# Kernel tuning notes

Measured on AMD Instinct MI355X. Metric: run time of the kernel, lower is better.

The kernel has to match this reference:

```python
import jax, jax.numpy as jnp
import numpy as np

NEG_INF_SCALE = -1e9  # matches mask * -1000000000.0 in the original


def setup_inputs() -> dict:
    key = jax.random.key(0)
    k1, k2, k3, k4 = jax.random.split(key, 4)
    B, H, S, D = 2, 16, 2048, 64
    return {
        "query": jax.random.normal(k1, (B, H, S, D), dtype=jnp.float32),
        "key": jax.random.normal(k2, (B, H, S, D), dtype=jnp.float32),
        "value": jax.random.normal(k3, (B, H, S, D), dtype=jnp.float32),
        "mask": jax.random.randint(k4, (B, 1, 1, S), 0, 2, dtype=jnp.int32),
    }


def reference(query, key, value, mask):
    head_dimension = query.shape[-1]
    scale = 1.0 / jnp.sqrt(jnp.float32(head_dimension))
    # (b h q d),(b h k d) -> (b h q k)
    logits = jnp.einsum("bhqd,bhkd->bhqk", query, key) * scale
    logits = logits + mask.astype(logits.dtype) * NEG_INF_SCALE
    attention_weights = jax.nn.softmax(logits, axis=-1)
    # (b h q k),(b h k d) -> (b h q d)
    output = jnp.einsum("bhqk,bhkd->bhqd", attention_weights, value)
    return output, attention_weights
```

## Files before the change

### kernel.cpp

```cpp
#include <hip/hip_runtime.h>

#define SEQ   2048
#define DIM   64
#define NB    2
#define NH    16
#define NHEAD (NB * NH)
#define BQ    128
#define BK    64
#define NKT   (SEQ / BK)
#define NQT   (SEQ / BQ)
#define QSCALE 0.18033688011112042f

typedef float  f32x4  __attribute__((ext_vector_type(4)));
typedef short  bf16x8 __attribute__((ext_vector_type(8)));
typedef short  s16x4  __attribute__((ext_vector_type(4)));
typedef unsigned short u16;
typedef u16    u16x8  __attribute__((ext_vector_type(8)));
typedef unsigned int u32x4 __attribute__((ext_vector_type(4)));

__device__ __forceinline__ short f2bf(float x) {
    unsigned u = __float_as_uint(x);
    return (short)((u + 0x7FFFu + ((u >> 16) & 1u)) >> 16);
}

__device__ __forceinline__ unsigned cvtpk(float lo, float hi) {
    unsigned r;
    asm("v_cvt_pk_bf16_f32 %0, %1, %2" : "=v"(r) : "v"(lo), "v"(hi));
    return r;
}

__device__ __forceinline__ void gll16(const void* g, void* l) {
    __builtin_amdgcn_global_load_lds(
        (const __attribute__((address_space(1))) unsigned int*)g,
        (__attribute__((address_space(3))) unsigned int*)l, 16, 0, 0);
}

__device__ __forceinline__ bf16x8 ldfrag_swz(const u16* tile, int row, int kbase) {
    const char* rp = (const char*)(tile + row * 64);
    const int sw = (row & 7) << 4;
    s16x4 lo = *reinterpret_cast<const s16x4*>(rp + (((kbase << 1)     ) ^ sw));
    s16x4 hi = *reinterpret_cast<const s16x4*>(rp + (((kbase << 1) + 32) ^ sw));
    bf16x8 f;
    f[0] = lo[0]; f[1] = lo[1]; f[2] = lo[2]; f[3] = lo[3];
    f[4] = hi[0]; f[5] = hi[1]; f[6] = hi[2]; f[7] = hi[3];
    return f;
}

__global__ __launch_bounds__(256)
void conv_k_kernel(const float* __restrict__ K, u16* __restrict__ Kp)
{
    const int idx = (int)blockIdx.x * 256 + (int)threadIdx.x;
    const int u  = idx & 7;
    const int r  = (idx >> 3) & 63;
    const int kt = (idx >> 9) & 31;
    const int h  = idx >> 14;
    const int d0 = ((u ^ (r & 7)) << 3);
    const float* src = K + (((size_t)h * SEQ + (size_t)kt * 64 + r) * DIM + d0);
    const float4 a = *reinterpret_cast<const float4*>(src);
    const float4 b = *reinterpret_cast<const float4*>(src + 4);
    u16x8 o;
    o[0] = (u16)f2bf(a.x); o[1] = (u16)f2bf(a.y); o[2] = (u16)f2bf(a.z); o[3] = (u16)f2bf(a.w);
    o[4] = (u16)f2bf(b.x); o[5] = (u16)f2bf(b.y); o[6] = (u16)f2bf(b.z); o[7] = (u16)f2bf(b.w);
    *reinterpret_cast<u16x8*>(Kp + (size_t)idx * 8) = o;
}

__global__ __launch_bounds__(256)
void conv_v_kernel(const float* __restrict__ V, u16* __restrict__ Vp)
{
    __shared__ float tile[64][65];
    const int tid = (int)threadIdx.x;
    const int h   = (int)blockIdx.x >> 5;
    const int kt  = (int)blockIdx.x & 31;

    const int row0 = tid >> 4;
    const int c0   = (tid & 15) << 2;
    #pragma unroll
    for (int i = 0; i < 4; ++i) {
        const int row = row0 + (i << 4);
        const float4 v = *reinterpret_cast<const float4*>(
            V + (((size_t)h * SEQ + (size_t)kt * 64 + row) * DIM + c0));
        tile[row][c0 + 0] = v.x; tile[row][c0 + 1] = v.y;
        tile[row][c0 + 2] = v.z; tile[row][c0 + 3] = v.w;
    }
    __syncthreads();

    #pragma unroll
    for (int i = 0; i < 2; ++i) {
        const int oi = tid + i * 256;
        const int u  = oi & 7;
        const int rd = oi >> 3;
        const int k0 = ((u ^ (rd & 7)) << 3);
        u16x8 o;
        #pragma unroll
        for (int j = 0; j < 8; ++j)
            o[j] = (u16)f2bf(tile[k0 + j][rd]);
        *reinterpret_cast<u16x8*>(Vp + ((size_t)((h * 32 + kt) * 512 + oi)) * 8) = o;
    }
}

__global__ __launch_bounds__(512, 4)
void sdpa_main_kernel(const float* __restrict__ Qp, const u16* __restrict__ Kp,
                      const u16* __restrict__ Vp, const int* __restrict__ Mp,
                      float* __restrict__ Op, float* __restrict__ Pg_)
{
    __shared__ u16   Ks[2][4096];
    __shared__ u16   Vs[2][4096];
    __shared__ float Fb[SEQ];

    const int tid  = (int)threadIdx.x;
    const int lane = tid & 63;
    const int w    = tid >> 6;
    const int mrow = lane & 15;
    const int kgrp = (lane >> 4) << 2;

    const int bid  = (int)blockIdx.x;
    const int xcd  = bid & 7;
    const int slot = bid >> 3;
    const int bh   = xcd * 4 + (slot >> 4);
    const int qt   = slot & 15;

    const size_t headoff = (size_t)bh * SEQ * DIM;
    const float* Qg = Qp + headoff + (size_t)qt * BQ * DIM;
    const u16*   Kh = Kp + (size_t)bh * NKT * 4096;
    const u16*   Vh = Vp + (size_t)bh * NKT * 4096;
    const int*   Mg = Mp + (size_t)(bh / NH) * SEQ;
    float*       Og = Op + headoff + (size_t)qt * BQ * DIM;
    float*       Pg = Pg_ + ((size_t)bh * SEQ + (size_t)qt * BQ) * SEQ;

    {
        const int4 m0 = *reinterpret_cast<const int4*>(Mg + tid * 4);
        float4 f0;
        f0.x = m0.x ? -1.0e9f : 0.0f; f0.y = m0.y ? -1.0e9f : 0.0f;
        f0.z = m0.z ? -1.0e9f : 0.0f; f0.w = m0.w ? -1.0e9f : 0.0f;
        *reinterpret_cast<float4*>(&Fb[tid * 4]) = f0;
    }

    bf16x8 qf0, qf1;
    {
        const float* qrow = Qg + (size_t)(w * 16 + mrow) * DIM;
        const float4 a = *reinterpret_cast<const float4*>(qrow + kgrp);
        const float4 b = *reinterpret_cast<const float4*>(qrow + 16 + kgrp);
        const float4 c = *reinterpret_cast<const float4*>(qrow + 32 + kgrp);
        const float4 d = *reinterpret_cast<const float4*>(qrow + 48 + kgrp);
        qf0[0] = f2bf(a.x * QSCALE); qf0[1] = f2bf(a.y * QSCALE);
        qf0[2] = f2bf(a.z * QSCALE); qf0[3] = f2bf(a.w * QSCALE);
        qf0[4] = f2bf(b.x * QSCALE); qf0[5] = f2bf(b.y * QSCALE);
        qf0[6] = f2bf(b.z * QSCALE); qf0[7] = f2bf(b.w * QSCALE);
        qf1[0] = f2bf(c.x * QSCALE); qf1[1] = f2bf(c.y * QSCALE);
        qf1[2] = f2bf(c.z * QSCALE); qf1[3] = f2bf(c.w * QSCALE);
        qf1[4] = f2bf(d.x * QSCALE); qf1[5] = f2bf(d.y * QSCALE);
        qf1[6] = f2bf(d.z * QSCALE); qf1[7] = f2bf(d.w * QSCALE);
    }
    __syncthreads();

    const int so = tid * 8;

    gll16(Kh + so, &Ks[0][so]);
    asm volatile("s_waitcnt vmcnt(0)" ::: "memory");
    __builtin_amdgcn_s_barrier();

    float lsum = 0.f;
    int cur = 0;

    for (int kt = 0; kt < NKT; ++kt) {
        gll16(Kh + (size_t)((kt + 1) & (NKT - 1)) * 4096 + so, &Ks[cur ^ 1][so]);
        asm volatile("s_waitcnt vmcnt(1)" ::: "memory");
        __builtin_amdgcn_s_barrier();
        __builtin_amdgcn_sched_barrier(0);

        const int k0 = kt * BK;
        #pragma unroll
        for (int t = 0; t < 4; ++t) {
            const bf16x8 kf0 = ldfrag_swz(Ks[cur], t * 16 + mrow, kgrp);
            const bf16x8 kf1 = ldfrag_swz(Ks[cur], t * 16 + mrow, 32 + kgrp);
            f32x4 a = {0.f, 0.f, 0.f, 0.f};
            a = __builtin_amdgcn_mfma_f32_16x16x32_bf16(kf0, qf0, a, 0, 0, 0);
            a = __builtin_amdgcn_mfma_f32_16x16x32_bf16(kf1, qf1, a, 0, 0, 0);
            const float4 b = *reinterpret_cast<const float4*>(&Fb[k0 + t * 16 + kgrp]);
            lsum += __builtin_amdgcn_exp2f(a[0] + b.x);
            lsum += __builtin_amdgcn_exp2f(a[1] + b.y);
            lsum += __builtin_amdgcn_exp2f(a[2] + b.z);
            lsum += __builtin_amdgcn_exp2f(a[3] + b.w);
        }

        asm volatile("s_waitcnt lgkmcnt(0)" ::: "memory");
        __builtin_amdgcn_s_barrier();
        cur ^= 1;
    }

    lsum += __shfl_xor(lsum, 16);
    lsum += __shfl_xor(lsum, 32);
    const float rinv = 1.0f / lsum;

    f32x4 oacc[4];
    #pragma unroll
    for (int n = 0; n < 4; ++n) {
        oacc[n][0] = 0.f; oacc[n][1] = 0.f; oacc[n][2] = 0.f; oacc[n][3] = 0.f;
    }

    gll16(Kh + so, &Ks[0][so]);
    gll16(Vh + so, &Vs[0][so]);
    asm volatile("s_waitcnt vmcnt(0)" ::: "memory");
    __builtin_amdgcn_s_barrier();
    cur = 0;

    float* prow = Pg + (size_t)(w * 16 + mrow) * SEQ + kgrp;

    for (int kt = 0; kt < NKT; ++kt) {
        {
            const size_t nt = (size_t)((kt + 1) & (NKT - 1)) * 4096;
            gll16(Kh + nt + so, &Ks[cur ^ 1][so]);
            gll16(Vh + nt + so, &Vs[cur ^ 1][so]);
        }
        asm volatile("s_waitcnt vmcnt(6)" ::: "memory");
        __builtin_amdgcn_s_barrier();
        __builtin_amdgcn_sched_barrier(0);

        const int k0 = kt * BK;
        bf16x8 pf0, pf1;

        #pragma unroll
        for (int half = 0; half < 2; ++half) {
            f32x4 p[2];
            #pragma unroll
            for (int i = 0; i < 2; ++i) {
                const int t = half * 2 + i;
                const bf16x8 kf0 = ldfrag_swz(Ks[cur], t * 16 + mrow, kgrp);
                const bf16x8 kf1 = ldfrag_swz(Ks[cur], t * 16 + mrow, 32 + kgrp);
                f32x4 a = {0.f, 0.f, 0.f, 0.f};
                a = __builtin_amdgcn_mfma_f32_16x16x32_bf16(kf0, qf0, a, 0, 0, 0);
                a = __builtin_amdgcn_mfma_f32_16x16x32_bf16(kf1, qf1, a, 0, 0, 0);
                const float4 b = *reinterpret_cast<const float4*>(&Fb[k0 + t * 16 + kgrp]);
                p[i][0] = __builtin_amdgcn_exp2f(a[0] + b.x) * rinv;
                p[i][1] = __builtin_amdgcn_exp2f(a[1] + b.y) * rinv;
                p[i][2] = __builtin_amdgcn_exp2f(a[2] + b.z) * rinv;
                p[i][3] = __builtin_amdgcn_exp2f(a[3] + b.w) * rinv;
                *reinterpret_cast<float4*>(prow + k0 + t * 16) =
                    *reinterpret_cast<const float4*>(&p[i]);
            }
            const u32x4 packed = { cvtpk(p[0][0], p[0][1]), cvtpk(p[0][2], p[0][3]),
                                   cvtpk(p[1][0], p[1][1]), cvtpk(p[1][2], p[1][3]) };
            if (half == 0) pf0 = __builtin_bit_cast(bf16x8, packed);
            else           pf1 = __builtin_bit_cast(bf16x8, packed);
        }

        #pragma unroll
        for (int n = 0; n < 4; ++n) {
            const bf16x8 vf0 = ldfrag_swz(Vs[cur], n * 16 + mrow, kgrp);
            const bf16x8 vf1 = ldfrag_swz(Vs[cur], n * 16 + mrow, 32 + kgrp);
            oacc[n] = __builtin_amdgcn_mfma_f32_16x16x32_bf16(pf0, vf0, oacc[n], 0, 0, 0);
            oacc[n] = __builtin_amdgcn_mfma_f32_16x16x32_bf16(pf1, vf1, oacc[n], 0, 0, 0);
        }

        asm volatile("s_waitcnt lgkmcnt(0)" ::: "memory");
        __builtin_amdgcn_s_barrier();
        cur ^= 1;
    }

    #pragma unroll
    for (int n = 0; n < 4; ++n) {
        #pragma unroll
        for (int r = 0; r < 4; ++r)
            Og[(size_t)(w * 16 + kgrp + r) * DIM + n * 16 + mrow] = oacc[n][r];
    }
}

extern "C" void kernel_launch(void* const* d_in, const int* in_sizes, int n_in,
                              void* d_out, int out_size, void* d_ws, size_t ws_size,
                              hipStream_t stream) {
    const float* Q = (const float*)d_in[0];
    const float* K = (const float*)d_in[1];
    const float* V = (const float*)d_in[2];
    const int*   M = (const int*)d_in[3];
    float* O = (float*)d_out;
    float* P = O + (size_t)NB * NH * SEQ * DIM;

    u16* Kp = (u16*)d_ws;
    u16* Vp = Kp + (size_t)NHEAD * SEQ * DIM;

    conv_k_kernel<<<dim3(NHEAD * NKT * 64 * 8 / 256), dim3(256), 0, stream>>>(K, Kp);
    conv_v_kernel<<<dim3(NHEAD * NKT), dim3(256), 0, stream>>>(V, Vp);

    sdpa_main_kernel<<<dim3(NHEAD * NQT), dim3(512, 1, 1), 0, stream>>>(Q, Kp, Vp, M, O, P);
}
```

Measured before the change: 193.2 us.

## Triple-buffer K/V tiles with two-ahead prefetch and nontemporal output stores

```diff
diff --git a/kernel.cpp b/kernel.cpp
--- a/kernel.cpp
+++ b/kernel.cpp
@@ -103,8 +103,8 @@
                       const u16* __restrict__ Vp, const int* __restrict__ Mp,
                       float* __restrict__ Op, float* __restrict__ Pg_)
 {
-    __shared__ u16   Ks[2][4096];
-    __shared__ u16   Vs[2][4096];
+    __shared__ u16   Ks[3][4096];
+    __shared__ u16   Vs[3][4096];
     __shared__ float Fb[SEQ];
 
     const int tid  = (int)threadIdx.x;
@@ -156,23 +156,24 @@
     const int so = tid * 8;
 
     gll16(Kh + so, &Ks[0][so]);
-    asm volatile("s_waitcnt vmcnt(0)" ::: "memory");
+    gll16(Kh + 4096 + so, &Ks[1][so]);
+    asm volatile("s_waitcnt vmcnt(1)" ::: "memory");
     __builtin_amdgcn_s_barrier();
 
     float lsum = 0.f;
-    int cur = 0;
+    int bcur = 0, bpre = 2;
 
     for (int kt = 0; kt < NKT; ++kt) {
-        gll16(Kh + (size_t)((kt + 1) & (NKT - 1)) * 4096 + so, &Ks[cur ^ 1][so]);
-        asm volatile("s_waitcnt vmcnt(1)" ::: "memory");
+        gll16(Kh + (size_t)((kt + 2) & (NKT - 1)) * 4096 + so, &Ks[bpre][so]);
+        asm volatile("s_waitcnt vmcnt(2)" ::: "memory");
         __builtin_amdgcn_s_barrier();
         __builtin_amdgcn_sched_barrier(0);
 
         const int k0 = kt * BK;
         #pragma unroll
         for (int t = 0; t < 4; ++t) {
-            const bf16x8 kf0 = ldfrag_swz(Ks[cur], t * 16 + mrow, kgrp);
-            const bf16x8 kf1 = ldfrag_swz(Ks[cur], t * 16 + mrow, 32 + kgrp);
+            const bf16x8 kf0 = ldfrag_swz(Ks[bcur], t * 16 + mrow, kgrp);
+            const bf16x8 kf1 = ldfrag_swz(Ks[bcur], t * 16 + mrow, 32 + kgrp);
             f32x4 a = {0.f, 0.f, 0.f, 0.f};
             a = __builtin_amdgcn_mfma_f32_16x16x32_bf16(kf0, qf0, a, 0, 0, 0);
             a = __builtin_amdgcn_mfma_f32_16x16x32_bf16(kf1, qf1, a, 0, 0, 0);
@@ -185,13 +186,18 @@
 
         asm volatile("s_waitcnt lgkmcnt(0)" ::: "memory");
         __builtin_amdgcn_s_barrier();
-        cur ^= 1;
-    }
+        bcur = (bcur == 2) ? 0 : bcur + 1;
+        bpre = (bpre == 2) ? 0 : bpre + 1;
+    }
+
+    asm volatile("s_waitcnt vmcnt(0)" ::: "memory");
 
     lsum += __shfl_xor(lsum, 16);
     lsum += __shfl_xor(lsum, 32);
     const float rinv = 1.0f / lsum;
 
+    __builtin_amdgcn_s_barrier();
+
     f32x4 oacc[4];
     #pragma unroll
     for (int n = 0; n < 4; ++n) {
@@ -200,19 +206,21 @@
 
     gll16(Kh + so, &Ks[0][so]);
     gll16(Vh + so, &Vs[0][so]);
-    asm volatile("s_waitcnt vmcnt(0)" ::: "memory");
+    gll16(Kh + 4096 + so, &Ks[1][so]);
+    gll16(Vh + 4096 + so, &Vs[1][so]);
+    asm volatile("s_waitcnt vmcnt(2)" ::: "memory");
     __builtin_amdgcn_s_barrier();
-    cur = 0;
+    bcur = 0; bpre = 2;
 
     float* prow = Pg + (size_t)(w * 16 + mrow) * SEQ + kgrp;
 
     for (int kt = 0; kt < NKT; ++kt) {
         {
-            const size_t nt = (size_t)((kt + 1) & (NKT - 1)) * 4096;
-            gll16(Kh + nt + so, &Ks[cur ^ 1][so]);
-            gll16(Vh + nt + so, &Vs[cur ^ 1][so]);
-        }
-        asm volatile("s_waitcnt vmcnt(6)" ::: "memory");
+            const size_t nt = (size_t)((kt + 2) & (NKT - 1)) * 4096;
+            gll16(Kh + nt + so, &Ks[bpre][so]);
+            gll16(Vh + nt + so, &Vs[bpre][so]);
+        }
+        asm volatile("s_waitcnt vmcnt(8)" ::: "memory");
         __builtin_amdgcn_s_barrier();
         __builtin_amdgcn_sched_barrier(0);
 
@@ -225,8 +233,8 @@
             #pragma unroll
             for (int i = 0; i < 2; ++i) {
                 const int t = half * 2 + i;
-                const bf16x8 kf0 = ldfrag_swz(Ks[cur], t * 16 + mrow, kgrp);
-                const bf16x8 kf1 = ldfrag_swz(Ks[cur], t * 16 + mrow, 32 + kgrp);
+                const bf16x8 kf0 = ldfrag_swz(Ks[bcur], t * 16 + mrow, kgrp);
+                const bf16x8 kf1 = ldfrag_swz(Ks[bcur], t * 16 + mrow, 32 + kgrp);
                 f32x4 a = {0.f, 0.f, 0.f, 0.f};
                 a = __builtin_amdgcn_mfma_f32_16x16x32_bf16(kf0, qf0, a, 0, 0, 0);
                 a = __builtin_amdgcn_mfma_f32_16x16x32_bf16(kf1, qf1, a, 0, 0, 0);
@@ -235,8 +243,8 @@
                 p[i][1] = __builtin_amdgcn_exp2f(a[1] + b.y) * rinv;
                 p[i][2] = __builtin_amdgcn_exp2f(a[2] + b.z) * rinv;
                 p[i][3] = __builtin_amdgcn_exp2f(a[3] + b.w) * rinv;
-                *reinterpret_cast<float4*>(prow + k0 + t * 16) =
-                    *reinterpret_cast<const float4*>(&p[i]);
+                __builtin_nontemporal_store(
+                    p[i], reinterpret_cast<f32x4*>(prow + k0 + t * 16));
             }
             const u32x4 packed = { cvtpk(p[0][0], p[0][1]), cvtpk(p[0][2], p[0][3]),
                                    cvtpk(p[1][0], p[1][1]), cvtpk(p[1][2], p[1][3]) };
@@ -246,22 +254,24 @@
 
         #pragma unroll
         for (int n = 0; n < 4; ++n) {
-            const bf16x8 vf0 = ldfrag_swz(Vs[cur], n * 16 + mrow, kgrp);
-            const bf16x8 vf1 = ldfrag_swz(Vs[cur], n * 16 + mrow, 32 + kgrp);
+            const bf16x8 vf0 = ldfrag_swz(Vs[bcur], n * 16 + mrow, kgrp);
+            const bf16x8 vf1 = ldfrag_swz(Vs[bcur], n * 16 + mrow, 32 + kgrp);
             oacc[n] = __builtin_amdgcn_mfma_f32_16x16x32_bf16(pf0, vf0, oacc[n], 0, 0, 0);
             oacc[n] = __builtin_amdgcn_mfma_f32_16x16x32_bf16(pf1, vf1, oacc[n], 0, 0, 0);
         }
 
         asm volatile("s_waitcnt lgkmcnt(0)" ::: "memory");
         __builtin_amdgcn_s_barrier();
-        cur ^= 1;
+        bcur = (bcur == 2) ? 0 : bcur + 1;
+        bpre = (bpre == 2) ? 0 : bpre + 1;
     }
 
     #pragma unroll
     for (int n = 0; n < 4; ++n) {
         #pragma unroll
         for (int r = 0; r < 4; ++r)
-            Og[(size_t)(w * 16 + kgrp + r) * DIM + n * 16 + mrow] = oacc[n][r];
+            __builtin_nontemporal_store(
+                oacc[n][r], &Og[(size_t)(w * 16 + kgrp + r) * DIM + n * 16 + mrow]);
     }
 }
 
```

Result: slower. 226.9 us (+17.4%).
